# Kernel tuning notes

Hardware: AMD Instinct MI355X
Metric: run time of the kernel (lower is better)

Reference implementation:

```python
import jax, jax.numpy as jnp
import numpy as np

N = 100000
E = 1600000
FEAT = 128
EMB = 64
HID = 64
OUT = 16


def _glorot(key, shape):
    fan_in, fan_out = shape[1], shape[0]
    lim = (6.0 / (fan_in + fan_out)) ** 0.5
    return jax.random.uniform(key, shape, jnp.float32, -lim, lim)


def setup_inputs() -> dict:
    key = jax.random.key(0)
    ks = jax.random.split(key, 16)
    return {
        "x_feat": jax.random.normal(ks[0], (N, FEAT), jnp.float32),
        "x_emb": jax.random.normal(ks[1], (N, 2, EMB), jnp.float32),
        "edge_index": jax.random.randint(ks[2], (2, E), 0, N, jnp.int32),
        # layer 0: SAGEConv(FEAT -> HID), Linear(EMB -> HID)
        "Wl0": _glorot(ks[3], (HID, FEAT)),
        "bl0": jnp.zeros((HID,), jnp.float32),
        "Wr0": _glorot(ks[4], (HID, FEAT)),
        "We0": _glorot(ks[5], (HID, EMB)),
        "be0": jnp.zeros((HID,), jnp.float32),
        # layer 1 (last): SAGEConv(HID -> OUT), Linear(EMB==HID -> OUT)
        "Wl1": _glorot(ks[6], (OUT, HID)),
        "bl1": jnp.zeros((OUT,), jnp.float32),
        "Wr1": _glorot(ks[7], (OUT, HID)),
        "We1": _glorot(ks[8], (OUT, HID)),
        "be1": jnp.zeros((OUT,), jnp.float32),
    }


def _sage_conv(x, edge_index, Wl, bl, Wr):
    # PyG SAGEConv with mean aggregation:
    #   out = lin_l(mean_{j in N(i)} x_j) + lin_r(x_i)
    src, dst = edge_index[0], edge_index[1]
    msg = x[src]                                   # [E, C] gather
    agg = jax.ops.segment_sum(msg, dst, num_segments=N)       # [N, C]
    deg = jax.ops.segment_sum(jnp.ones((E,), x.dtype), dst, num_segments=N)
    agg = agg / jnp.maximum(deg, 1.0)[:, None]     # mean over neighbors
    return agg @ Wl.T + bl + x @ Wr.T


def reference(x_feat, x_emb, edge_index,
              Wl0, bl0, Wr0, We0, be0,
              Wl1, bl1, Wr1, We1, be1):
    # forward(x=(x_feat, x_emb), edge_index=...) path, eval mode (dropout p=0)
    e = x_emb.mean(axis=1)                         # [N, EMB]
    # layer 0 (all but last): relu(sage + linear(emb))
    h = _sage_conv(x_feat, edge_index, Wl0, bl0, Wr0)
    e = e @ We0.T + be0
    h = jax.nn.relu(h + e)
    # last layer: no relu
    h = _sage_conv(h, edge_index, Wl1, bl1, Wr1)
    e = e @ We1.T + be1
    return h + e
```

## Files before the change

### kernel.cpp

```cpp
#include <hip/hip_runtime.h>
#include <hip/hip_bf16.h>
#include <cstddef>

#define NN 100000
#define EE 1600000
#define NPB 128
#define NB  782
#define ECH 4096
#define NCH 391
#define CAP 6144

typedef __attribute__((ext_vector_type(8))) short bf16x8;
typedef __attribute__((ext_vector_type(8))) unsigned short u16x8;
typedef __attribute__((ext_vector_type(4))) float f32x4;

#define Y0S 72
#define RES 68

static inline int ceil_div(int a, int b){ return (a + b - 1) / b; }

__device__ inline unsigned short f2bf(float f){
  union { float f; unsigned u; } v; v.f = f;
  unsigned r = (v.u + 0x7fff + ((v.u >> 16) & 1)) >> 16;
  return (unsigned short)r;
}
__device__ inline float bf2f(unsigned short s){
  union { unsigned u; float f; } v; v.u = ((unsigned)s) << 16;
  return v.f;
}

__global__ void prep_all_kernel(const float* __restrict__ Wl0, const float* __restrict__ Wr0,
                                const float* __restrict__ We0, const float* __restrict__ bl0,
                                const float* __restrict__ be0, const float* __restrict__ We1,
                                const float* __restrict__ be1,
                                unsigned short* __restrict__ wcat, float* __restrict__ wee,
                                float* __restrict__ b1e, float* __restrict__ bias0){
  int idx = blockIdx.x * blockDim.x + threadIdx.x;
  if (idx < 128 * 192){
    int n = idx / 192, k = idx % 192;
    float v;
    if (n < 64) v = (k < 128) ? Wl0[n * 128 + k] : 0.f;
    else        v = (k < 128) ? Wr0[(n - 64) * 128 + k] : We0[(n - 64) * 64 + (k - 128)];
    wcat[idx] = f2bf(v);
  } else if (idx < 128 * 192 + 16 * 64){
    int j = idx - 128 * 192;
    int i = j >> 6, c = j & 63;
    float s = 0.f;
    for (int k = 0; k < 64; k++) s += We1[i * 64 + k] * We0[k * 64 + c];
    wee[j] = s;
  } else if (idx < 128 * 192 + 16 * 64 + 16){
    int i = idx - (128 * 192 + 16 * 64);
    float s = be1[i];
    for (int k = 0; k < 64; k++) s += We1[i * 64 + k] * be0[k];
    b1e[i] = s;
  } else if (idx < 128 * 192 + 16 * 64 + 16 + 64){
    int i = idx - (128 * 192 + 16 * 64 + 16);
    bias0[i] = bl0[i] + be0[i];
  }
}

__global__ __launch_bounds__(256) void escatter_kernel(const int* __restrict__ src,
                                                       const int* __restrict__ dst,
                                                       int* __restrict__ cur,
                                                       int* __restrict__ ebkt){
  __shared__ int lh[NB];
  __shared__ int lo[NB];
  int t = threadIdx.x;
  int e0 = blockIdx.x * ECH;
  int ne = EE - e0; if (ne > ECH) ne = ECH;
  for (int i = t; i < NB; i += 256) lh[i] = 0;
  __syncthreads();
  for (int i = t; i < ne; i += 256)
    atomicAdd(&lh[dst[e0 + i] >> 7], 1);
  __syncthreads();
  for (int i = t; i < NB; i += 256){
    int c = lh[i];
    lo[i] = c ? atomicAdd(&cur[i], c) : 0;
    lh[i] = 0;
  }
  __syncthreads();
  for (int i = t; i < ne; i += 256){
    int d = dst[e0 + i], b = d >> 7;
    int r = atomicAdd(&lh[b], 1);
    int p = lo[b] + r;
    if (p < CAP) ebkt[b * CAP + p] = ((d & 127) << 24) | src[e0 + i];
  }
}

__global__ __launch_bounds__(256) void bsort_kernel(
    const int* __restrict__ cur, int* __restrict__ ebkt,
    int* __restrict__ rs, int* __restrict__ deg){
  __shared__ int lraw[CAP];
  __shared__ int lout[CAP];
  __shared__ int lh[NPB];
  __shared__ int loff[NPB];
  __shared__ int lcur[NPB];
  const int t = threadIdx.x;
  const int b = blockIdx.x;
  const int e0 = b * CAP;
  int cnt = cur[b];
  if (cnt > CAP) cnt = CAP;
  for (int i = t; i < NPB; i += 256) lh[i] = 0;
  __syncthreads();
  for (int i = t; i < cnt; i += 256){
    int w = ebkt[e0 + i];
    lraw[i] = w;
    atomicAdd(&lh[((unsigned)w) >> 24], 1);
  }
  __syncthreads();
  {
    int v = (t < NPB) ? lh[t] : 0;
    int s = v;
    for (int off = 1; off < NPB; off <<= 1){
      int x = 0;
      if (t < NPB && t >= off) x = loff[t - off];
      __syncthreads();
      if (t < NPB) loff[t] = s;
      __syncthreads();
      if (t < NPB && t >= off) s += loff[t - off];
      __syncthreads();
    }
    if (t < NPB){ loff[t] = s - v; lcur[t] = s - v; }
  }
  __syncthreads();
  for (int i = t; i < cnt; i += 256){
    int w = lraw[i];
    int d = ((unsigned)w) >> 24;
    int pos = atomicAdd(&lcur[d], 1);
    lout[pos] = w & 0xFFFFFF;
  }
  __syncthreads();
  for (int i = t; i < cnt; i += 256) ebkt[e0 + i] = lout[i];
  if (t < NPB){
    int node = b * NPB + t;
    if (node < NN){
      rs[node]  = e0 + loff[t];
      deg[node] = lh[t];
    }
  }
}

__global__ __launch_bounds__(256, 3) void l0_gemm_kernel(
    const float* __restrict__ x_feat, const float* __restrict__ x_emb,
    const unsigned short* __restrict__ wcat,
    unsigned short* __restrict__ y0g, float* __restrict__ re0g,
    unsigned short* __restrict__ e_bf, int M){
  __shared__ unsigned short As[64 * 200];
  __shared__ unsigned short Ys[64 * Y0S];
  __shared__ float          Rs[64 * RES];
  const int t = threadIdx.x;
  const int row0 = blockIdx.x * 64;
  float4 tmpa[12], tmpb[12];
  #pragma unroll
  for (int k = 0; k < 12; k++){
    int idx = t + k * 256;
    int r = idx / 48, q = idx % 48;
    int row = row0 + r;
    float4 v = make_float4(0.f, 0.f, 0.f, 0.f);
    float4 u = make_float4(0.f, 0.f, 0.f, 0.f);
    if (row < M){
      if (q < 32) v = ((const float4*)x_feat)[(size_t)row * 32 + q];
      else {
        v = ((const float4*)x_emb)[(size_t)row * 32 + (q - 32)];
        u = ((const float4*)x_emb)[(size_t)row * 32 + 16 + (q - 32)];
      }
    }
    tmpa[k] = v; tmpb[k] = u;
  }
  #pragma unroll
  for (int k = 0; k < 12; k++){
    int idx = t + k * 256;
    int r = idx / 48, q = idx % 48;
    int row = row0 + r;
    float4 v = tmpa[k];
    if (q >= 32){
      float4 u = tmpb[k];
      v.x = 0.5f * (v.x + u.x); v.y = 0.5f * (v.y + u.y);
      v.z = 0.5f * (v.z + u.z); v.w = 0.5f * (v.w + u.w);
    }
    ushort4 s; s.x = f2bf(v.x); s.y = f2bf(v.y); s.z = f2bf(v.z); s.w = f2bf(v.w);
    *(ushort4*)&As[r * 200 + q * 4] = s;
    if (q >= 32 && row < M)
      *(ushort4*)&e_bf[(size_t)row * 64 + (q - 32) * 4] = s;
  }
  const int w = t >> 6, l = t & 63;
  const int lm = l & 15, quad = l >> 4;
  bf16x8 bfr0[6], bfr1[6];
  {
    int n0 = w * 16 + lm;
    int n1 = 64 + w * 16 + lm;
    #pragma unroll
    for (int ks = 0; ks < 6; ks++){
      bfr0[ks] = *(const bf16x8*)&wcat[n0 * 192 + ks * 32 + quad * 8];
      bfr1[ks] = *(const bf16x8*)&wcat[n1 * 192 + ks * 32 + quad * 8];
    }
  }
  __syncthreads();
  for (int rg = 0; rg < 4; rg++){
    bf16x8 af[6];
    #pragma unroll
    for (int ks = 0; ks < 6; ks++)
      af[ks] = *(const bf16x8*)&As[(rg * 16 + lm) * 200 + ks * 32 + quad * 8];
    f32x4 acc0 = {0.f, 0.f, 0.f, 0.f};
    f32x4 acc1 = {0.f, 0.f, 0.f, 0.f};
    #pragma unroll
    for (int ks = 0; ks < 6; ks++){
      acc0 = __builtin_amdgcn_mfma_f32_16x16x32_bf16(af[ks], bfr0[ks], acc0, 0, 0, 0);
      acc1 = __builtin_amdgcn_mfma_f32_16x16x32_bf16(af[ks], bfr1[ks], acc1, 0, 0, 0);
    }
    #pragma unroll
    for (int r = 0; r < 4; r++){
      int lrow = rg * 16 + quad * 4 + r;
      Ys[lrow * Y0S + w * 16 + lm] = f2bf(acc0[r]);
      Rs[lrow * RES + w * 16 + lm] = acc1[r];
    }
  }
  __syncthreads();
  #pragma unroll
  for (int k = 0; k < 2; k++){
    int idx = t + k * 256;
    int r = idx >> 3, c8 = idx & 7;
    int grow = row0 + r;
    if (grow < M){
      u16x8 v = *(const u16x8*)&Ys[r * Y0S + c8 * 8];
      *(u16x8*)&y0g[(size_t)grow * 64 + c8 * 8] = v;
    }
  }
  #pragma unroll
  for (int k = 0; k < 4; k++){
    int idx = t + k * 256;
    int r = idx >> 4, c4 = idx & 15;
    int grow = row0 + r;
    if (grow < M){
      f32x4 v = *(const f32x4*)&Rs[r * RES + c4 * 4];
      *(f32x4*)&re0g[(size_t)grow * 64 + c4 * 4] = v;
    }
  }
}

__global__ void agg0_kernel(const unsigned short* __restrict__ y0,
                            const float4* __restrict__ re0,
                            const float* __restrict__ bias0,
                            const int* __restrict__ rs, const int* __restrict__ deg,
                            const int* __restrict__ ssrc, unsigned short* __restrict__ h){
  int g = blockIdx.x * blockDim.x + threadIdx.x;
  if (g >= NN * 16) return;
  int node = g >> 4, lane = g & 15;
  int start = rs[node], cnt = deg[node];
  float acc[4][4] = {};
  int i = 0;
  for (; i + 8 <= cnt; i += 8){
    int s[8];
    #pragma unroll
    for (int j = 0; j < 8; j++) s[j] = ssrc[start + i + j];
    ushort4 v[8];
    #pragma unroll
    for (int j = 0; j < 8; j++) v[j] = *(const ushort4*)&y0[(size_t)s[j] * 64 + lane * 4];
    #pragma unroll
    for (int j = 0; j < 8; j++){
      acc[j & 3][0] += bf2f(v[j].x); acc[j & 3][1] += bf2f(v[j].y);
      acc[j & 3][2] += bf2f(v[j].z); acc[j & 3][3] += bf2f(v[j].w);
    }
  }
  for (; i + 4 <= cnt; i += 4){
    int s[4];
    #pragma unroll
    for (int j = 0; j < 4; j++) s[j] = ssrc[start + i + j];
    #pragma unroll
    for (int j = 0; j < 4; j++){
      ushort4 v = *(const ushort4*)&y0[(size_t)s[j] * 64 + lane * 4];
      acc[j][0] += bf2f(v.x); acc[j][1] += bf2f(v.y);
      acc[j][2] += bf2f(v.z); acc[j][3] += bf2f(v.w);
    }
  }
  for (; i < cnt; i++){
    int s = ssrc[start + i];
    ushort4 v = *(const ushort4*)&y0[(size_t)s * 64 + lane * 4];
    acc[0][0] += bf2f(v.x); acc[0][1] += bf2f(v.y); acc[0][2] += bf2f(v.z); acc[0][3] += bf2f(v.w);
  }
  float sx = (acc[0][0] + acc[1][0]) + (acc[2][0] + acc[3][0]);
  float sy = (acc[0][1] + acc[1][1]) + (acc[2][1] + acc[3][1]);
  float sz = (acc[0][2] + acc[1][2]) + (acc[2][2] + acc[3][2]);
  float sw = (acc[0][3] + acc[1][3]) + (acc[2][3] + acc[3][3]);
  float inv = 1.0f / (float)(cnt > 1 ? cnt : 1);
  float4 rv = re0[(size_t)node * 16 + lane];
  float4 bb = ((const float4*)bias0)[lane];
  float vx = sx * inv + rv.x + bb.x;
  float vy = sy * inv + rv.y + bb.y;
  float vz = sz * inv + rv.z + bb.z;
  float vw = sw * inv + rv.w + bb.w;
  vx = vx > 0.f ? vx : 0.f;
  vy = vy > 0.f ? vy : 0.f;
  vz = vz > 0.f ? vz : 0.f;
  vw = vw > 0.f ? vw : 0.f;
  ushort4 o; o.x = f2bf(vx); o.y = f2bf(vy); o.z = f2bf(vz); o.w = f2bf(vw);
  *(ushort4*)&h[(size_t)node * 64 + lane * 4] = o;
}

__global__ __launch_bounds__(256) void gemm16_dual_kernel(
    const unsigned short* __restrict__ H, const unsigned short* __restrict__ E,
    const float* __restrict__ Wl1, const float* __restrict__ Wr1,
    const float* __restrict__ wee,
    const float* __restrict__ bl1, const float* __restrict__ b1e,
    unsigned short* __restrict__ Y1, float* __restrict__ Out, int M){
  __shared__ float Hs[64][65];
  __shared__ float Es[64][65];
  __shared__ float Wls[16][65];
  __shared__ float Wrs[16][65];
  __shared__ float Wes[16][65];
  __shared__ float bs[16];
  const int t = threadIdx.x;
  const int row0 = blockIdx.x * 64;
  {
    int j = t >> 4, kq = t & 15;
    float4 a = ((const float4*)Wl1)[j * 16 + kq];
    float4 b = ((const float4*)Wr1)[j * 16 + kq];
    float4 c = ((const float4*)wee)[j * 16 + kq];
    Wls[j][kq*4+0]=a.x; Wls[j][kq*4+1]=a.y; Wls[j][kq*4+2]=a.z; Wls[j][kq*4+3]=a.w;
    Wrs[j][kq*4+0]=b.x; Wrs[j][kq*4+1]=b.y; Wrs[j][kq*4+2]=b.z; Wrs[j][kq*4+3]=b.w;
    Wes[j][kq*4+0]=c.x; Wes[j][kq*4+1]=c.y; Wes[j][kq*4+2]=c.z; Wes[j][kq*4+3]=c.w;
  }
  if (t < 16) bs[t] = bl1[t] + b1e[t];
  for (int idx = t; idx < 64 * 16; idx += 256){
    int n = idx >> 4, kq = idx & 15;
    int row = row0 + n;
    ushort4 hv = make_ushort4(0,0,0,0), ev = make_ushort4(0,0,0,0);
    if (row < M){
      hv = *(const ushort4*)&H[(size_t)row * 64 + kq * 4];
      ev = *(const ushort4*)&E[(size_t)row * 64 + kq * 4];
    }
    Hs[n][kq*4+0]=bf2f(hv.x); Hs[n][kq*4+1]=bf2f(hv.y); Hs[n][kq*4+2]=bf2f(hv.z); Hs[n][kq*4+3]=bf2f(hv.w);
    Es[n][kq*4+0]=bf2f(ev.x); Es[n][kq*4+1]=bf2f(ev.y); Es[n][kq*4+2]=bf2f(ev.z); Es[n][kq*4+3]=bf2f(ev.w);
  }
  __syncthreads();
  const int n = t >> 2, jq = t & 3;
  float y[4] = {}, o[4] = {};
  #pragma unroll 4
  for (int k = 0; k < 64; k++){
    float a = Hs[n][k];
    float e = Es[n][k];
    #pragma unroll
    for (int j = 0; j < 4; j++){
      y[j] = fmaf(a, Wls[jq*4 + j][k], y[j]);
      o[j] = fmaf(a, Wrs[jq*4 + j][k], o[j]);
      o[j] = fmaf(e, Wes[jq*4 + j][k], o[j]);
    }
  }
  int row = row0 + n;
  if (row < M){
    ushort4 yb; yb.x = f2bf(y[0]); yb.y = f2bf(y[1]); yb.z = f2bf(y[2]); yb.w = f2bf(y[3]);
    *(ushort4*)&Y1[(size_t)row * 16 + jq * 4] = yb;
    ((float4*)Out)[(size_t)row * 4 + jq] =
        make_float4(o[0] + bs[jq*4+0], o[1] + bs[jq*4+1], o[2] + bs[jq*4+2], o[3] + bs[jq*4+3]);
  }
}

__global__ void agg1_kernel(const unsigned short* __restrict__ y1,
                            const int* __restrict__ rs, const int* __restrict__ deg,
                            const int* __restrict__ ssrc, float4* __restrict__ outp){
  int g = blockIdx.x * blockDim.x + threadIdx.x;
  if (g >= NN * 4) return;
  int node = g >> 2, lane = g & 3;
  int start = rs[node], cnt = deg[node];
  float acc[4][4] = {};
  int i = 0;
  for (; i + 8 <= cnt; i += 8){
    int s[8];
    #pragma unroll
    for (int j = 0; j < 8; j++) s[j] = ssrc[start + i + j];
    ushort4 v[8];
    #pragma unroll
    for (int j = 0; j < 8; j++) v[j] = *(const ushort4*)&y1[(size_t)s[j] * 16 + lane * 4];
    #pragma unroll
    for (int j = 0; j < 8; j++){
      acc[j & 3][0] += bf2f(v[j].x); acc[j & 3][1] += bf2f(v[j].y);
      acc[j & 3][2] += bf2f(v[j].z); acc[j & 3][3] += bf2f(v[j].w);
    }
  }
  for (; i + 4 <= cnt; i += 4){
    int s[4];
    #pragma unroll
    for (int j = 0; j < 4; j++) s[j] = ssrc[start + i + j];
    #pragma unroll
    for (int j = 0; j < 4; j++){
      ushort4 v = *(const ushort4*)&y1[(size_t)s[j] * 16 + lane * 4];
      acc[j][0] += bf2f(v.x); acc[j][1] += bf2f(v.y);
      acc[j][2] += bf2f(v.z); acc[j][3] += bf2f(v.w);
    }
  }
  for (; i < cnt; i++){
    int s = ssrc[start + i];
    ushort4 v = *(const ushort4*)&y1[(size_t)s * 16 + lane * 4];
    acc[0][0] += bf2f(v.x); acc[0][1] += bf2f(v.y); acc[0][2] += bf2f(v.z); acc[0][3] += bf2f(v.w);
  }
  float sx = (acc[0][0] + acc[1][0]) + (acc[2][0] + acc[3][0]);
  float sy = (acc[0][1] + acc[1][1]) + (acc[2][1] + acc[3][1]);
  float sz = (acc[0][2] + acc[1][2]) + (acc[2][2] + acc[3][2]);
  float sw = (acc[0][3] + acc[1][3]) + (acc[2][3] + acc[3][3]);
  float inv = 1.0f / (float)(cnt > 1 ? cnt : 1);
  float4 o = outp[(size_t)node * 4 + lane];
  o.x += sx * inv;
  o.y += sy * inv;
  o.z += sz * inv;
  o.w += sw * inv;
  outp[(size_t)node * 4 + lane] = o;
}

extern "C" void kernel_launch(void* const* d_in, const int* in_sizes, int n_in,
                              void* d_out, int out_size, void* d_ws, size_t ws_size,
                              hipStream_t stream){
  (void)in_sizes; (void)n_in; (void)out_size; (void)ws_size;
  const float* x_feat = (const float*)d_in[0];
  const float* x_emb  = (const float*)d_in[1];
  const int*   ei     = (const int*)d_in[2];
  const float* Wl0 = (const float*)d_in[3];
  const float* bl0 = (const float*)d_in[4];
  const float* Wr0 = (const float*)d_in[5];
  const float* We0 = (const float*)d_in[6];
  const float* be0 = (const float*)d_in[7];
  const float* Wl1 = (const float*)d_in[8];
  const float* bl1 = (const float*)d_in[9];
  const float* Wr1 = (const float*)d_in[10];
  const float* We1 = (const float*)d_in[11];
  const float* be1 = (const float*)d_in[12];
  float* out = (float*)d_out;

  char* w = (char*)d_ws;
  float* re0   = (float*)w;                  w += sizeof(float) * (size_t)NN * 64;
  unsigned short* h   = (unsigned short*)w;  w += sizeof(unsigned short) * (size_t)NN * 64;
  unsigned short* y0  = (unsigned short*)w;  w += sizeof(unsigned short) * (size_t)NN * 64;
  unsigned short* e_bf= (unsigned short*)w;  w += sizeof(unsigned short) * (size_t)NN * 64;
  unsigned short* y1  = (unsigned short*)w;  w += sizeof(unsigned short) * (size_t)NN * 16;
  unsigned short* wcat= (unsigned short*)w;  w += sizeof(unsigned short) * 128 * 192;
  float* wee   = (float*)w;                  w += sizeof(float) * 16 * 64;
  float* b1e   = (float*)w;                  w += sizeof(float) * 16;
  float* bias0 = (float*)w;                  w += sizeof(float) * 64;
  int* ebkt    = (int*)w;                    w += sizeof(int) * (size_t)NB * CAP;
  int* cur     = (int*)w;                    w += sizeof(int) * NB;
  int* rs      = (int*)w;                    w += sizeof(int) * NN;
  int* deg     = (int*)w;                    w += sizeof(int) * NN;

  const int* srcp = ei;
  const int* dstp = ei + EE;

  hipMemsetAsync(cur, 0, sizeof(int) * NB, stream);

  prep_all_kernel<<<ceil_div(128*192 + 16*64 + 16 + 64, 256), 256, 0, stream>>>(
      Wl0, Wr0, We0, bl0, be0, We1, be1, wcat, wee, b1e, bias0);

  escatter_kernel<<<NCH, 256, 0, stream>>>(srcp, dstp, cur, ebkt);
  bsort_kernel<<<NB, 256, 0, stream>>>(cur, ebkt, rs, deg);

  l0_gemm_kernel<<<ceil_div(NN, 64), 256, 0, stream>>>(x_feat, x_emb, wcat, y0, re0, e_bf, NN);

  agg0_kernel<<<ceil_div(NN * 16, 256), 256, 0, stream>>>(
      y0, (const float4*)re0, bias0, rs, deg, ebkt, h);

  gemm16_dual_kernel<<<ceil_div(NN, 64), 256, 0, stream>>>(h, e_bf, Wl1, Wr1, wee,
                                                           bl1, b1e, y1, out, NN);
  agg1_kernel<<<ceil_div(NN * 4, 256), 256, 0, stream>>>(y1, rs, deg, ebkt, (float4*)out);
}
```

Measured before the change: 315.9 us.

## Store re0 in bf16, widen gather loads, alias LDS, fold memset into prep

Several changes at once. The layer-0 root term re0 is now stored in bf16 instead of fp32, which halves its write and read traffic. The GEMM kernel reuses the A-tile shared memory for its output staging so it can raise occupancy to 4 blocks, and the aggregation kernels use 8-wide bf16 loads per thread, with fewer threads per node and no 4-edge remainder loop. The bucket counter memset is folded into the prep kernel and the per-bucket capacity is reduced. These trade some precision in re0 and risk overflowing buckets if any bucket exceeds the smaller capacity.

```diff
diff --git a/kernel.cpp b/kernel.cpp
--- a/kernel.cpp
+++ b/kernel.cpp
@@ -8,14 +8,13 @@
 #define NB  782
 #define ECH 4096
 #define NCH 391
-#define CAP 6144
+#define CAP 4096
 
 typedef __attribute__((ext_vector_type(8))) short bf16x8;
 typedef __attribute__((ext_vector_type(8))) unsigned short u16x8;
 typedef __attribute__((ext_vector_type(4))) float f32x4;
 
-#define Y0S 72
-#define RES 68
+#define YTS 72
 
 static inline int ceil_div(int a, int b){ return (a + b - 1) / b; }
 
@@ -29,33 +28,41 @@
   return v.f;
 }
 
+#define PRE_W (128 * 192)
+#define PRE_E (PRE_W + 16 * 64)
+#define PRE_B (PRE_E + 16)
+#define PRE_C (PRE_B + 64)
+#define PRE_N (PRE_C + NB)
 __global__ void prep_all_kernel(const float* __restrict__ Wl0, const float* __restrict__ Wr0,
                                 const float* __restrict__ We0, const float* __restrict__ bl0,
                                 const float* __restrict__ be0, const float* __restrict__ We1,
                                 const float* __restrict__ be1,
                                 unsigned short* __restrict__ wcat, float* __restrict__ wee,
-                                float* __restrict__ b1e, float* __restrict__ bias0){
+                                float* __restrict__ b1e, float* __restrict__ bias0,
+                                int* __restrict__ cur){
   int idx = blockIdx.x * blockDim.x + threadIdx.x;
-  if (idx < 128 * 192){
+  if (idx < PRE_W){
     int n = idx / 192, k = idx % 192;
     float v;
     if (n < 64) v = (k < 128) ? Wl0[n * 128 + k] : 0.f;
     else        v = (k < 128) ? Wr0[(n - 64) * 128 + k] : We0[(n - 64) * 64 + (k - 128)];
     wcat[idx] = f2bf(v);
-  } else if (idx < 128 * 192 + 16 * 64){
-    int j = idx - 128 * 192;
+  } else if (idx < PRE_E){
+    int j = idx - PRE_W;
     int i = j >> 6, c = j & 63;
     float s = 0.f;
     for (int k = 0; k < 64; k++) s += We1[i * 64 + k] * We0[k * 64 + c];
     wee[j] = s;
-  } else if (idx < 128 * 192 + 16 * 64 + 16){
-    int i = idx - (128 * 192 + 16 * 64);
+  } else if (idx < PRE_B){
+    int i = idx - PRE_E;
     float s = be1[i];
     for (int k = 0; k < 64; k++) s += We1[i * 64 + k] * be0[k];
     b1e[i] = s;
-  } else if (idx < 128 * 192 + 16 * 64 + 16 + 64){
-    int i = idx - (128 * 192 + 16 * 64 + 16);
+  } else if (idx < PRE_C){
+    int i = idx - PRE_B;
     bias0[i] = bl0[i] + be0[i];
+  } else if (idx < PRE_N){
+    cur[idx - PRE_C] = 0;
   }
 }
 
@@ -140,14 +147,15 @@
   }
 }
 
-__global__ __launch_bounds__(256, 3) void l0_gemm_kernel(
+__global__ __launch_bounds__(256, 4) void l0_gemm_kernel(
     const float* __restrict__ x_feat, const float* __restrict__ x_emb,
     const unsigned short* __restrict__ wcat,
-    unsigned short* __restrict__ y0g, float* __restrict__ re0g,
+    unsigned short* __restrict__ y0g, unsigned short* __restrict__ re0g,
     unsigned short* __restrict__ e_bf, int M){
-  __shared__ unsigned short As[64 * 200];
-  __shared__ unsigned short Ys[64 * Y0S];
-  __shared__ float          Rs[64 * RES];
+  __shared__ unsigned short smem[64 * 200];
+  unsigned short* As = smem;
+  unsigned short* Ys = smem;
+  unsigned short* Rs = smem + 64 * YTS;
   const int t = threadIdx.x;
   const int row0 = blockIdx.x * 64;
   float4 tmpa[12], tmpb[12];
@@ -196,6 +204,8 @@
     }
   }
   __syncthreads();
+  f32x4 a0[4], a1[4];
+  #pragma unroll
   for (int rg = 0; rg < 4; rg++){
     bf16x8 af[6];
     #pragma unroll
@@ -208,11 +218,16 @@
       acc0 = __builtin_amdgcn_mfma_f32_16x16x32_bf16(af[ks], bfr0[ks], acc0, 0, 0, 0);
       acc1 = __builtin_amdgcn_mfma_f32_16x16x32_bf16(af[ks], bfr1[ks], acc1, 0, 0, 0);
     }
+    a0[rg] = acc0; a1[rg] = acc1;
+  }
+  __syncthreads();
+  #pragma unroll
+  for (int rg = 0; rg < 4; rg++){
     #pragma unroll
     for (int r = 0; r < 4; r++){
       int lrow = rg * 16 + quad * 4 + r;
-      Ys[lrow * Y0S + w * 16 + lm] = f2bf(acc0[r]);
-      Rs[lrow * RES + w * 16 + lm] = acc1[r];
+      Ys[lrow * YTS + w * 16 + lm] = f2bf(a0[rg][r]);
+      Rs[lrow * YTS + w * 16 + lm] = f2bf(a1[rg][r]);
     }
   }
   __syncthreads();
@@ -222,79 +237,54 @@
     int r = idx >> 3, c8 = idx & 7;
     int grow = row0 + r;
     if (grow < M){
-      u16x8 v = *(const u16x8*)&Ys[r * Y0S + c8 * 8];
-      *(u16x8*)&y0g[(size_t)grow * 64 + c8 * 8] = v;
-    }
-  }
-  #pragma unroll
-  for (int k = 0; k < 4; k++){
-    int idx = t + k * 256;
-    int r = idx >> 4, c4 = idx & 15;
-    int grow = row0 + r;
-    if (grow < M){
-      f32x4 v = *(const f32x4*)&Rs[r * RES + c4 * 4];
-      *(f32x4*)&re0g[(size_t)grow * 64 + c4 * 4] = v;
+      *(u16x8*)&y0g[(size_t)grow * 64 + c8 * 8]  = *(const u16x8*)&Ys[r * YTS + c8 * 8];
+      *(u16x8*)&re0g[(size_t)grow * 64 + c8 * 8] = *(const u16x8*)&Rs[r * YTS + c8 * 8];
     }
   }
 }
 
 __global__ void agg0_kernel(const unsigned short* __restrict__ y0,
-                            const float4* __restrict__ re0,
+                            const unsigned short* __restrict__ re0,
                             const float* __restrict__ bias0,
                             const int* __restrict__ rs, const int* __restrict__ deg,
                             const int* __restrict__ ssrc, unsigned short* __restrict__ h){
   int g = blockIdx.x * blockDim.x + threadIdx.x;
-  if (g >= NN * 16) return;
-  int node = g >> 4, lane = g & 15;
+  if (g >= NN * 8) return;
+  int node = g >> 3, lane = g & 7;
   int start = rs[node], cnt = deg[node];
-  float acc[4][4] = {};
+  float acc[4][8] = {};
   int i = 0;
   for (; i + 8 <= cnt; i += 8){
     int s[8];
     #pragma unroll
     for (int j = 0; j < 8; j++) s[j] = ssrc[start + i + j];
-    ushort4 v[8];
-    #pragma unroll
-    for (int j = 0; j < 8; j++) v[j] = *(const ushort4*)&y0[(size_t)s[j] * 64 + lane * 4];
-    #pragma unroll
-    for (int j = 0; j < 8; j++){
-      acc[j & 3][0] += bf2f(v[j].x); acc[j & 3][1] += bf2f(v[j].y);
-      acc[j & 3][2] += bf2f(v[j].z); acc[j & 3][3] += bf2f(v[j].w);
-    }
-  }
-  for (; i + 4 <= cnt; i += 4){
-    int s[4];
-    #pragma unroll
-    for (int j = 0; j < 4; j++) s[j] = ssrc[start + i + j];
-    #pragma unroll
-    for (int j = 0; j < 4; j++){
-      ushort4 v = *(const ushort4*)&y0[(size_t)s[j] * 64 + lane * 4];
-      acc[j][0] += bf2f(v.x); acc[j][1] += bf2f(v.y);
-      acc[j][2] += bf2f(v.z); acc[j][3] += bf2f(v.w);
-    }
+    u16x8 v[8];
+    #pragma unroll
+    for (int j = 0; j < 8; j++) v[j] = *(const u16x8*)&y0[(size_t)s[j] * 64 + lane * 8];
+    #pragma unroll
+    for (int j = 0; j < 8; j++)
+      #pragma unroll
+      for (int k = 0; k < 8; k++) acc[j & 3][k] += bf2f((unsigned short)v[j][k]);
   }
   for (; i < cnt; i++){
     int s = ssrc[start + i];
-    ushort4 v = *(const ushort4*)&y0[(size_t)s * 64 + lane * 4];
-    acc[0][0] += bf2f(v.x); acc[0][1] += bf2f(v.y); acc[0][2] += bf2f(v.z); acc[0][3] += bf2f(v.w);
-  }
-  float sx = (acc[0][0] + acc[1][0]) + (acc[2][0] + acc[3][0]);
-  float sy = (acc[0][1] + acc[1][1]) + (acc[2][1] + acc[3][1]);
-  float sz = (acc[0][2] + acc[1][2]) + (acc[2][2] + acc[3][2]);
-  float sw = (acc[0][3] + acc[1][3]) + (acc[2][3] + acc[3][3]);
+    u16x8 v = *(const u16x8*)&y0[(size_t)s * 64 + lane * 8];
+    #pragma unroll
+    for (int k = 0; k < 8; k++) acc[0][k] += bf2f((unsigned short)v[k]);
+  }
   float inv = 1.0f / (float)(cnt > 1 ? cnt : 1);
-  float4 rv = re0[(size_t)node * 16 + lane];
-  float4 bb = ((const float4*)bias0)[lane];
-  float vx = sx * inv + rv.x + bb.x;
-  float vy = sy * inv + rv.y + bb.y;
-  float vz = sz * inv + rv.z + bb.z;
-  float vw = sw * inv + rv.w + bb.w;
-  vx = vx > 0.f ? vx : 0.f;
-  vy = vy > 0.f ? vy : 0.f;
-  vz = vz > 0.f ? vz : 0.f;
-  vw = vw > 0.f ? vw : 0.f;
-  ushort4 o; o.x = f2bf(vx); o.y = f2bf(vy); o.z = f2bf(vz); o.w = f2bf(vw);
-  *(ushort4*)&h[(size_t)node * 64 + lane * 4] = o;
+  u16x8 rv = *(const u16x8*)&re0[(size_t)node * 64 + lane * 8];
+  float4 ba = ((const float4*)bias0)[lane * 2];
+  float4 bb = ((const float4*)bias0)[lane * 2 + 1];
+  float bv[8] = {ba.x, ba.y, ba.z, ba.w, bb.x, bb.y, bb.z, bb.w};
+  u16x8 o;
+  #pragma unroll
+  for (int k = 0; k < 8; k++){
+    float sum = (acc[0][k] + acc[1][k]) + (acc[2][k] + acc[3][k]);
+    float x = sum * inv + bf2f((unsigned short)rv[k]) + bv[k];
+    o[k] = f2bf(x > 0.f ? x : 0.f);
+  }
+  *(u16x8*)&h[(size_t)node * 64 + lane * 8] = o;
 }
 
 __global__ __launch_bounds__(256) void gemm16_dual_kernel(
@@ -357,53 +347,41 @@
 
 __global__ void agg1_kernel(const unsigned short* __restrict__ y1,
                             const int* __restrict__ rs, const int* __restrict__ deg,
-                            const int* __restrict__ ssrc, float4* __restrict__ outp){
+                            const int* __restrict__ ssrc, float* __restrict__ outp){
   int g = blockIdx.x * blockDim.x + threadIdx.x;
-  if (g >= NN * 4) return;
-  int node = g >> 2, lane = g & 3;
+  if (g >= NN * 2) return;
+  int node = g >> 1, lane = g & 1;
   int start = rs[node], cnt = deg[node];
-  float acc[4][4] = {};
+  float acc[4][8] = {};
   int i = 0;
   for (; i + 8 <= cnt; i += 8){
     int s[8];
     #pragma unroll
     for (int j = 0; j < 8; j++) s[j] = ssrc[start + i + j];
-    ushort4 v[8];
-    #pragma unroll
-    for (int j = 0; j < 8; j++) v[j] = *(const ushort4*)&y1[(size_t)s[j] * 16 + lane * 4];
-    #pragma unroll
-    for (int j = 0; j < 8; j++){
-      acc[j & 3][0] += bf2f(v[j].x); acc[j & 3][1] += bf2f(v[j].y);
-      acc[j & 3][2] += bf2f(v[j].z); acc[j & 3][3] += bf2f(v[j].w);
-    }
-  }
-  for (; i + 4 <= cnt; i += 4){
-    int s[4];
-    #pragma unroll
-    for (int j = 0; j < 4; j++) s[j] = ssrc[start + i + j];
-    #pragma unroll
-    for (int j = 0; j < 4; j++){
-      ushort4 v = *(const ushort4*)&y1[(size_t)s[j] * 16 + lane * 4];
-      acc[j][0] += bf2f(v.x); acc[j][1] += bf2f(v.y);
-      acc[j][2] += bf2f(v.z); acc[j][3] += bf2f(v.w);
-    }
+    u16x8 v[8];
+    #pragma unroll
+    for (int j = 0; j < 8; j++) v[j] = *(const u16x8*)&y1[(size_t)s[j] * 16 + lane * 8];
+    #pragma unroll
+    for (int j = 0; j < 8; j++)
+      #pragma unroll
+      for (int k = 0; k < 8; k++) acc[j & 3][k] += bf2f((unsigned short)v[j][k]);
   }
   for (; i < cnt; i++){
     int s = ssrc[start + i];
-    ushort4 v = *(const ushort4*)&y1[(size_t)s * 16 + lane * 4];
-    acc[0][0] += bf2f(v.x); acc[0][1] += bf2f(v.y); acc[0][2] += bf2f(v.z); acc[0][3] += bf2f(v.w);
-  }
-  float sx = (acc[0][0] + acc[1][0]) + (acc[2][0] + acc[3][0]);
-  float sy = (acc[0][1] + acc[1][1]) + (acc[2][1] + acc[3][1]);
-  float sz = (acc[0][2] + acc[1][2]) + (acc[2][2] + acc[3][2]);
-  float sw = (acc[0][3] + acc[1][3]) + (acc[2][3] + acc[3][3]);
+    u16x8 v = *(const u16x8*)&y1[(size_t)s * 16 + lane * 8];
+    #pragma unroll
+    for (int k = 0; k < 8; k++) acc[0][k] += bf2f((unsigned short)v[k]);
+  }
   float inv = 1.0f / (float)(cnt > 1 ? cnt : 1);
-  float4 o = outp[(size_t)node * 4 + lane];
-  o.x += sx * inv;
-  o.y += sy * inv;
-  o.z += sz * inv;
-  o.w += sw * inv;
-  outp[(size_t)node * 4 + lane] = o;
+  f32x4 o0 = *(f32x4*)&outp[(size_t)node * 16 + lane * 8];
+  f32x4 o1 = *(f32x4*)&outp[(size_t)node * 16 + lane * 8 + 4];
+  #pragma unroll
+  for (int k = 0; k < 4; k++){
+    o0[k] += ((acc[0][k] + acc[1][k]) + (acc[2][k] + acc[3][k])) * inv;
+    o1[k] += ((acc[0][k+4] + acc[1][k+4]) + (acc[2][k+4] + acc[3][k+4])) * inv;
+  }
+  *(f32x4*)&outp[(size_t)node * 16 + lane * 8]     = o0;
+  *(f32x4*)&outp[(size_t)node * 16 + lane * 8 + 4] = o1;
 }
 
 extern "C" void kernel_launch(void* const* d_in, const int* in_sizes, int n_in,
@@ -426,7 +404,7 @@
   float* out = (float*)d_out;
 
   char* w = (char*)d_ws;
-  float* re0   = (float*)w;                  w += sizeof(float) * (size_t)NN * 64;
+  unsigned short* re0 = (unsigned short*)w;  w += sizeof(unsigned short) * (size_t)NN * 64;
   unsigned short* h   = (unsigned short*)w;  w += sizeof(unsigned short) * (size_t)NN * 64;
   unsigned short* y0  = (unsigned short*)w;  w += sizeof(unsigned short) * (size_t)NN * 64;
   unsigned short* e_bf= (unsigned short*)w;  w += sizeof(unsigned short) * (size_t)NN * 64;
@@ -443,20 +421,18 @@
   const int* srcp = ei;
   const int* dstp = ei + EE;
 
-  hipMemsetAsync(cur, 0, sizeof(int) * NB, stream);
-
-  prep_all_kernel<<<ceil_div(128*192 + 16*64 + 16 + 64, 256), 256, 0, stream>>>(
-      Wl0, Wr0, We0, bl0, be0, We1, be1, wcat, wee, b1e, bias0);
+  prep_all_kernel<<<ceil_div(PRE_N, 256), 256, 0, stream>>>(
+      Wl0, Wr0, We0, bl0, be0, We1, be1, wcat, wee, b1e, bias0, cur);
 
   escatter_kernel<<<NCH, 256, 0, stream>>>(srcp, dstp, cur, ebkt);
   bsort_kernel<<<NB, 256, 0, stream>>>(cur, ebkt, rs, deg);
 
   l0_gemm_kernel<<<ceil_div(NN, 64), 256, 0, stream>>>(x_feat, x_emb, wcat, y0, re0, e_bf, NN);
 
-  agg0_kernel<<<ceil_div(NN * 16, 256), 256, 0, stream>>>(
-      y0, (const float4*)re0, bias0, rs, deg, ebkt, h);
+  agg0_kernel<<<ceil_div(NN * 8, 256), 256, 0, stream>>>(
+      y0, re0, bias0, rs, deg, ebkt, h);
 
   gemm16_dual_kernel<<<ceil_div(NN, 64), 256, 0, stream>>>(h, e_bf, Wl1, Wr1, wee,
                                                            bl1, b1e, y1, out, NN);
-  agg1_kernel<<<ceil_div(NN * 4, 256), 256, 0, stream>>>(y1, rs, deg, ebkt, (float4*)out);
-}
+  agg1_kernel<<<ceil_div(NN * 2, 256), 256, 0, stream>>>(y1, rs, deg, ebkt, out);
+}
```

Result: slower. 328.4 us (+3.9%).
